# Kernel tuning notes

Hardware: AMD Instinct MI355X
Metric: run time of the kernel (lower is better)

Reference implementation:

```python
import jax, jax.numpy as jnp
import numpy as np

EMBED = 1024
HEADS = 16
HIDDEN = 4 * EMBED
EPS = 1e-5


def layer_norm(x, g, b):
    mu = jnp.mean(x, axis=-1, keepdims=True)
    var = jnp.var(x, axis=-1, keepdims=True)
    return (x - mu) * jax.lax.rsqrt(var + EPS) * g + b


def setup_inputs() -> dict:
    key = jax.random.key(0)
    ks = jax.random.split(key, 8)
    s = EMBED ** -0.5
    return {
        "x": jax.random.normal(ks[0], (4, 2048, EMBED), dtype=jnp.float32),
        "ln1_g": jnp.ones((EMBED,), jnp.float32),
        "ln1_b": jnp.zeros((EMBED,), jnp.float32),
        "qkv_w": jax.random.normal(ks[1], (3 * EMBED, EMBED), jnp.float32) * s,
        "out_w": jax.random.normal(ks[2], (EMBED, EMBED), jnp.float32) * s,
        "out_b": jnp.zeros((EMBED,), jnp.float32),
        "ln2_g": jnp.ones((EMBED,), jnp.float32),
        "ln2_b": jnp.zeros((EMBED,), jnp.float32),
        "fc1_w": jax.random.normal(ks[3], (HIDDEN, EMBED), jnp.float32) * s,
        "fc1_b": jnp.zeros((HIDDEN,), jnp.float32),
        "fc2_w": jax.random.normal(ks[4], (EMBED, HIDDEN), jnp.float32) * (HIDDEN ** -0.5),
        "fc2_b": jnp.zeros((EMBED,), jnp.float32),
    }


def reference(x, ln1_g, ln1_b, qkv_w, out_w, out_b, ln2_g, ln2_b, fc1_w, fc1_b, fc2_w, fc2_b):
    B, N, C = x.shape
    hd = C // HEADS
    # --- attention (pre-LN); note: NO 1/sqrt(d) scaling, matching the source ---
    h = layer_norm(x, ln1_g, ln1_b)
    qkv = h @ qkv_w.T                                  # [B,N,3C]
    qkv = qkv.reshape(B, N, 3, HEADS, hd).transpose(2, 0, 3, 1, 4)
    q, k, v = qkv[0], qkv[1], qkv[2]                   # [B,H,N,hd]
    attn = jax.nn.softmax(jnp.einsum("bhqd,bhkd->bhqk", q, k), axis=-1)
    o = jnp.einsum("bhqk,bhkd->bhqd", attn, v)
    o = o.transpose(0, 2, 1, 3).reshape(B, N, C)
    x = x + o @ out_w.T + out_b
    # --- MLP (exact erf GELU, matching nn.GELU default) ---
    h = layer_norm(x, ln2_g, ln2_b)
    h = jax.nn.gelu(h @ fc1_w.T + fc1_b, approximate=False)
    x = x + h @ fc2_w.T + fc2_b
    return x
```

## Files before the change

### kernel.cpp

```cpp
#include <hip/hip_runtime.h>
#include <cstdint>


using short8 = __attribute__((ext_vector_type(8))) short;
using f32x4  = __attribute__((ext_vector_type(4))) float;
using f32x16 = __attribute__((ext_vector_type(16))) float;

#define EMBED  1024
#define HIDDEN 4096
#define SEQ    2048
#define NTOK   8192

__device__ __forceinline__ ushort f2bf(float x) {
  union { float f; uint32_t u; } v; v.f = x;
  uint32_t r = v.u + 0x7fffu + ((v.u >> 16) & 1u);
  return (ushort)(r >> 16);
}

__device__ __forceinline__ uint32_t pkbf(float lo, float hi) {
  uint32_t r;
  asm("v_cvt_pk_bf16_f32 %0, %1, %2" : "=v"(r) : "v"(lo), "v"(hi));
  return r;
}

__device__ __forceinline__ void gload16(const void* g, void* l) {
  __builtin_amdgcn_global_load_lds((__attribute__((address_space(1))) void*)(g),
                                   (__attribute__((address_space(3))) void*)(l), 16, 0, 0);
}

template<int N> __device__ __forceinline__ void vwait() {
  asm volatile("s_waitcnt vmcnt(%0)" :: "n"(N) : "memory");
}
__device__ __forceinline__ void fence_bar() {
  asm volatile("" ::: "memory");
  __builtin_amdgcn_s_barrier();
  asm volatile("" ::: "memory");
}

__device__ __forceinline__ f32x4 mfma16(short8 a, short8 b, f32x4 c) {
  return __builtin_amdgcn_mfma_f32_16x16x32_bf16(a, b, c, 0, 0, 0);
}
__device__ __forceinline__ f32x16 mfma32(short8 a, short8 b, f32x16 c) {
  return __builtin_amdgcn_mfma_f32_32x32x16_bf16(a, b, c, 0, 0, 0);
}
__device__ __forceinline__ f32x16 zero16() {
  f32x16 z = {0.f,0.f,0.f,0.f,0.f,0.f,0.f,0.f,0.f,0.f,0.f,0.f,0.f,0.f,0.f,0.f};
  return z;
}

__global__ __launch_bounds__(256) void cvt_bf16_kernel(const float* __restrict__ in,
                                                       ushort* __restrict__ out, int n4) {
  int i = blockIdx.x * 256 + threadIdx.x;
  if (i < n4) {
    float4 v = reinterpret_cast<const float4*>(in)[i];
    ushort4 o; o.x = f2bf(v.x); o.y = f2bf(v.y); o.z = f2bf(v.z); o.w = f2bf(v.w);
    reinterpret_cast<ushort4*>(out)[i] = o;
  }
}

__global__ __launch_bounds__(256) void ln_kernel(const float* __restrict__ x,
                                                 const float* __restrict__ g,
                                                 const float* __restrict__ b,
                                                 ushort* __restrict__ out) {
  const int row = blockIdx.x, tid = threadIdx.x;
  const float4 xv = reinterpret_cast<const float4*>(x + (size_t)row * EMBED)[tid];
  float s  = xv.x + xv.y + xv.z + xv.w;
  float s2 = xv.x*xv.x + xv.y*xv.y + xv.z*xv.z + xv.w*xv.w;
  #pragma unroll
  for (int off = 32; off >= 1; off >>= 1) { s += __shfl_xor(s, off); s2 += __shfl_xor(s2, off); }
  __shared__ float ps[4], ps2[4];
  if ((tid & 63) == 0) { ps[tid >> 6] = s; ps2[tid >> 6] = s2; }
  __syncthreads();
  s  = ps[0] + ps[1] + ps[2] + ps[3];
  s2 = ps2[0] + ps2[1] + ps2[2] + ps2[3];
  const float mu  = s * (1.f / EMBED);
  const float var = s2 * (1.f / EMBED) - mu * mu;
  const float rs  = rsqrtf(var + 1e-5f);
  const float4 gv = reinterpret_cast<const float4*>(g)[tid];
  const float4 bv = reinterpret_cast<const float4*>(b)[tid];
  ushort4 o;
  o.x = f2bf((xv.x - mu) * rs * gv.x + bv.x);
  o.y = f2bf((xv.y - mu) * rs * gv.y + bv.y);
  o.z = f2bf((xv.z - mu) * rs * gv.z + bv.z);
  o.w = f2bf((xv.w - mu) * rs * gv.w + bv.w);
  reinterpret_cast<ushort4*>(out + (size_t)row * EMBED)[tid] = o;
}

template<int EPI, bool SQ>
__global__ __launch_bounds__(512) void gemm256(const ushort* __restrict__ A,
                                               const ushort* __restrict__ B,
                                               const float* __restrict__ bias,
                                               const float* __restrict__ res,
                                               ushort* __restrict__ outb,
                                               float* __restrict__ outf,
                                               int M, int N, int K, int gx) {
  constexpr int BN   = SQ ? 256 : 128;
  constexpr int MP   = SQ ? 8 : 4;
  constexpr int NPH  = SQ ? 2 : 1;
  constexpr int LPT  = SQ ? 4 : 3;
  constexpr int NB   = LPT - 2;
  constexpr int ABUF = 256 * 32;
  constexpr int BBUF = BN * 32;
  __shared__ ushort lds[4][ABUF + BBUF];

  const int nwg = gridDim.x;
  const int b0  = blockIdx.x;
  const int p = b0 & 7, li = b0 >> 3;
  int mt, nt;
  if ((gx & 7) == 0) {
    const int g = gx >> 3;
    mt = p * g + (li % g);
    nt = li / g;
  } else {
    const int g = (nwg / gx) >> 3;
    nt = p * g + (li % g);
    mt = li / g;
  }
  const int m0 = mt * 256;
  const int n0 = nt * BN;

  const int tid = threadIdx.x, lane = tid & 63, wave = tid >> 6;
  const int wm = (SQ ? (wave >> 2) : (wave >> 1)) * (MP * 16);
  const int wn = (SQ ? (wave & 3) : (wave & 1)) * 64;
  const int l15 = lane & 15, l4 = lane >> 4;
  const int NT = K >> 5;

  const ushort* aSrc[2];
  const ushort* bSrc[NB];
  #pragma unroll
  for (int rd = 0; rd < 2; ++rd) {
    const int slot = rd * 512 + tid;
    const int r = slot >> 2;
    const int cs = (slot & 3) ^ ((r >> 1) & 3);
    aSrc[rd] = A + (size_t)(m0 + r) * K + cs * 8;
  }
  #pragma unroll
  for (int rd = 0; rd < NB; ++rd) {
    const int slot = rd * 512 + tid;
    const int r = slot >> 2;
    const int cs = (slot & 3) ^ ((r >> 1) & 3);
    bSrc[rd] = B + (size_t)(n0 + r) * K + cs * 8;
  }
  auto stageA = [&](int buf, int rd) { gload16(aSrc[rd], &lds[buf][(rd * 512 + tid) * 8]); };
  auto stageB = [&](int buf, int rd) { gload16(bSrc[rd], &lds[buf][ABUF + (rd * 512 + tid) * 8]); };
  auto advance = [&]() {
    #pragma unroll
    for (int rd = 0; rd < 2; ++rd) aSrc[rd] += 32;
    #pragma unroll
    for (int rd = 0; rd < NB; ++rd) bSrc[rd] += 32;
  };

  #pragma unroll
  for (int t = 0; t < 3; ++t) {
    stageA(t, 0); stageA(t, 1);
    #pragma unroll
    for (int rd = 0; rd < NB; ++rd) stageB(t, rd);
    advance();
  }
  vwait<2 * LPT>();
  fence_bar();

  f32x4 acc[MP][4] = {};

  auto doTile = [&](int q, bool st, int wsel) {
    const ushort* bA = &lds[q][0];
    const ushort* bB = &lds[q][ABUF];
    const int sbuf = (q + 3) & 3;
    short8 bf[4];
    #pragma unroll
    for (int j = 0; j < 4; ++j) {
      const int rb = wn + j * 16 + l15;
      bf[j] = *reinterpret_cast<const short8*>(&bB[rb * 32 + ((l4 ^ ((rb >> 1) & 3)) * 8)]);
    }
    #pragma unroll
    for (int ph = 0; ph < NPH; ++ph) {
      short8 af[4];
      #pragma unroll
      for (int i = 0; i < 4; ++i) {
        const int ra = wm + (ph * 4 + i) * 16 + l15;
        af[i] = *reinterpret_cast<const short8*>(&bA[ra * 32 + ((l4 ^ ((ra >> 1) & 3)) * 8)]);
      }
      if (st) {
        if constexpr (SQ) {
          if (ph == 0) { stageA(sbuf, 0); stageA(sbuf, 1); }
          else         { stageB(sbuf, 0); stageB(sbuf, 1); }
        } else {
          stageA(sbuf, 0); stageA(sbuf, 1); stageB(sbuf, 0);
        }
      }
      fence_bar();
      __builtin_amdgcn_s_setprio(1);
      #pragma unroll
      for (int i = 0; i < 4; ++i)
        #pragma unroll
        for (int j = 0; j < 4; ++j)
          acc[ph * 4 + i][j] = mfma16(af[i], bf[j], acc[ph * 4 + i][j]);
      __builtin_amdgcn_s_setprio(0);
      if (ph == NPH - 1) {
        if (st) advance();
        if (wsel == 0)      vwait<2 * LPT>();
        else if (wsel == 1) vwait<LPT>();
        else if (wsel == 2) vwait<0>();
      }
      fence_bar();
    }
  };

  for (int u0 = 0; u0 < NT - 4; u0 += 4) {
    doTile(0, true, 0); doTile(1, true, 0); doTile(2, true, 0); doTile(3, true, 0);
  }
  doTile(0, true, 0); doTile(1, false, 1); doTile(2, false, 2); doTile(3, false, 3);

  #pragma unroll
  for (int i = 0; i < MP; ++i)
    #pragma unroll
    for (int j = 0; j < 4; ++j)
      #pragma unroll
      for (int r = 0; r < 4; ++r) {
        const int row = m0 + wm + i * 16 + l4 * 4 + r;
        const int col = n0 + wn + j * 16 + l15;
        const size_t idx = (size_t)row * N + col;
        float v = acc[i][j][r];
        if constexpr (EPI == 0) {
          outb[idx] = f2bf(v);
        } else if constexpr (EPI == 1) {
          outf[idx] = v + bias[col] + res[idx];
        } else {
          v += bias[col];
          v = 0.5f * v * (1.f + erff(v * 0.70710678118654752f));
          outb[idx] = f2bf(v);
        }
      }
}

#define KVB 64
#define NTT (SEQ / KVB)

__global__ __launch_bounds__(256, 2) void attn_kernel(const ushort* __restrict__ qk,
                                                      const ushort* __restrict__ vt,
                                                      ushort* __restrict__ outp) {
  const int tid = threadIdx.x, lane = tid & 63, wq = tid >> 6;
  const int hi = lane >> 5, lo = lane & 31;
  const int b = blockIdx.x >> 4, h = blockIdx.x & 15;
  const int q0 = blockIdx.y * 256;

  __shared__ ushort sK[2][64 * 64];
  __shared__ ushort sVt[2][64 * 64];
  __shared__ float sBc[4][2][32];

  short8 qf[2][4];
  #pragma unroll
  for (int s = 0; s < 2; ++s)
    #pragma unroll
    for (int kc = 0; kc < 4; ++kc)
      qf[s][kc] = *reinterpret_cast<const short8*>(
          qk + (size_t)(b * SEQ + q0 + wq * 64 + s * 32 + lo) * 2048 + h * 64 + kc * 16 + hi * 8);

  auto STAGE = [&](int bb, int kt) {
    #pragma unroll
    for (int i = 0; i < 2; ++i) {
      const int slot = i * 256 + tid;
      const int r = slot >> 3;
      const int c = (slot & 7) ^ (r & 7);
      gload16(qk + (size_t)(b * SEQ + kt + r) * 2048 + 1024 + h * 64 + c * 8,
              &sK[bb][(i * 256 + wq * 64) * 8]);
      gload16(vt + (size_t)(h * 64 + r) * 8192 + b * SEQ + kt + c * 8,
              &sVt[bb][(i * 256 + wq * 64) * 8]);
    }
  };

  f32x16 acc[2][2];
  #pragma unroll
  for (int s = 0; s < 2; ++s) { acc[s][0] = zero16(); acc[s][1] = zero16(); }
  float mst[2] = {-1e30f, -1e30f}, lst[2] = {0.f, 0.f};

  STAGE(0, 0);
  for (int t = 0; t < NTT; ++t) {
    const int cur = t & 1;
    __syncthreads();
    if (t + 1 < NTT) STAGE(cur ^ 1, (t + 1) * KVB);

    short8 kf[2][4];
    #pragma unroll
    for (int kvb = 0; kvb < 2; ++kvb)
      #pragma unroll
      for (int kc = 0; kc < 4; ++kc) {
        const int row = kvb * 32 + lo, ch = kc * 2 + hi;
        kf[kvb][kc] = *reinterpret_cast<const short8*>(
            &sK[cur][(row * 8 + (ch ^ (row & 7))) * 8]);
      }

    short8 pa[2][4];
    #pragma unroll
    for (int s = 0; s < 2; ++s) {
      f32x16 st[2];
      #pragma unroll
      for (int kvb = 0; kvb < 2; ++kvb) {
        f32x16 tq = zero16();
        tq = mfma32(kf[kvb][0], qf[s][0], tq);
        tq = mfma32(kf[kvb][1], qf[s][1], tq);
        tq = mfma32(kf[kvb][2], qf[s][2], tq);
        tq = mfma32(kf[kvb][3], qf[s][3], tq);
        st[kvb] = tq;
      }
      float pm = fmaxf(st[0][0], st[0][1]);
      #pragma unroll
      for (int r = 2; r < 16; ++r) pm = fmaxf(pm, st[0][r]);
      #pragma unroll
      for (int r = 0; r < 16; ++r) pm = fmaxf(pm, st[1][r]);
      pm = fmaxf(pm, __shfl_xor(pm, 32));
      if (__any(pm > mst[s] + 8.f)) {
        const float mn = fmaxf(mst[s], pm);
        const float al = __expf(mst[s] - mn);
        mst[s] = mn; lst[s] *= al;
        sBc[wq][s][lo] = al;
        asm volatile("s_waitcnt lgkmcnt(0)" ::: "memory");
        #pragma unroll
        for (int g = 0; g < 4; ++g) {
          const f32x4 a4 = *reinterpret_cast<const f32x4*>(&sBc[wq][s][g * 8 + hi * 4]);
          #pragma unroll
          for (int j = 0; j < 4; ++j) {
            acc[s][0][g * 4 + j] *= a4[j];
            acc[s][1][g * 4 + j] *= a4[j];
          }
        }
      }
      #pragma unroll
      for (int kvb = 0; kvb < 2; ++kvb)
        #pragma unroll
        for (int r = 0; r < 16; ++r)
          st[kvb][r] = __expf(st[kvb][r] - mst[s]);
      {
        const f32x16 sv = st[0] + st[1];
        float sum = ((sv[0] + sv[1]) + (sv[2] + sv[3])) + ((sv[4] + sv[5]) + (sv[6] + sv[7]))
                  + ((sv[8] + sv[9]) + (sv[10] + sv[11])) + ((sv[12] + sv[13]) + (sv[14] + sv[15]));
        sum += __shfl_xor(sum, 32);
        lst[s] += sum;
      }
      #pragma unroll
      for (int kvb = 0; kvb < 2; ++kvb)
        #pragma unroll
        for (int f = 0; f < 2; ++f) {
          uint32_t wa = pkbf(st[kvb][f * 8 + 0], st[kvb][f * 8 + 1]);
          uint32_t wb = pkbf(st[kvb][f * 8 + 2], st[kvb][f * 8 + 3]);
          uint32_t wc = pkbf(st[kvb][f * 8 + 4], st[kvb][f * 8 + 5]);
          uint32_t wd = pkbf(st[kvb][f * 8 + 6], st[kvb][f * 8 + 7]);
          asm volatile("v_permlane32_swap_b32 %0, %1" : "+v"(wa), "+v"(wc));
          asm volatile("v_permlane32_swap_b32 %0, %1" : "+v"(wb), "+v"(wd));
          union { uint32_t w[4]; short8 v; } u;
          u.w[0] = wa; u.w[1] = wb; u.w[2] = wc; u.w[3] = wd;
          pa[s][kvb * 2 + f] = u.v;
        }
    }

    #pragma unroll
    for (int db = 0; db < 2; ++db) {
      short8 vb[4];
      #pragma unroll
      for (int k4 = 0; k4 < 4; ++k4) {
        const int row = db * 32 + lo, ch = k4 * 2 + hi;
        vb[k4] = *reinterpret_cast<const short8*>(
            &sVt[cur][(row * 8 + (ch ^ (row & 7))) * 8]);
      }
      #pragma unroll
      for (int s = 0; s < 2; ++s) {
        acc[s][db] = mfma32(pa[s][0], vb[0], acc[s][db]);
        acc[s][db] = mfma32(pa[s][1], vb[1], acc[s][db]);
        acc[s][db] = mfma32(pa[s][2], vb[2], acc[s][db]);
        acc[s][db] = mfma32(pa[s][3], vb[3], acc[s][db]);
      }
    }
  }

  #pragma unroll
  for (int s = 0; s < 2; ++s) sBc[wq][s][lo] = 1.f / lst[s];
  asm volatile("s_waitcnt lgkmcnt(0)" ::: "memory");
  #pragma unroll
  for (int s = 0; s < 2; ++s)
    #pragma unroll
    for (int g = 0; g < 4; ++g) {
      const f32x4 r4 = *reinterpret_cast<const f32x4*>(&sBc[wq][s][g * 8 + hi * 4]);
      #pragma unroll
      for (int j = 0; j < 4; ++j) {
        const int qrow = q0 + wq * 64 + s * 32 + g * 8 + hi * 4 + j;
        #pragma unroll
        for (int db = 0; db < 2; ++db)
          outp[(size_t)(b * SEQ + qrow) * EMBED + h * 64 + db * 32 + lo] =
              f2bf(acc[s][db][g * 4 + j] * r4[j]);
      }
    }
}

extern "C" void kernel_launch(void* const* d_in, const int* in_sizes, int n_in,
                              void* d_out, int out_size, void* d_ws, size_t ws_size,
                              hipStream_t stream) {
  const float* x     = (const float*)d_in[0];
  const float* ln1_g = (const float*)d_in[1];
  const float* ln1_b = (const float*)d_in[2];
  const float* qkv_w = (const float*)d_in[3];
  const float* out_w = (const float*)d_in[4];
  const float* out_b = (const float*)d_in[5];
  const float* ln2_g = (const float*)d_in[6];
  const float* ln2_b = (const float*)d_in[7];
  const float* fc1_w = (const float*)d_in[8];
  const float* fc1_b = (const float*)d_in[9];
  const float* fc2_w = (const float*)d_in[10];
  const float* fc2_b = (const float*)d_in[11];
  float* out = (float*)d_out;
  char* ws = (char*)d_ws;

  ushort* qkvw = (ushort*)(ws);
  ushort* outw = (ushort*)(ws + 6291456);
  ushort* fc1w = (ushort*)(ws + 8388608);
  ushort* fc2w = (ushort*)(ws + 16777216);
  float*  x1   = (float*) (ws + 25165824);
  ushort* hbuf = (ushort*)(ws + 58720256);
  ushort* qkbuf= (ushort*)(ws + 75497472);
  ushort* vtbuf= (ushort*)(ws + 109051904);
  ushort* obuf = (ushort*)(ws + 125829120);
  ushort* gbuf = qkbuf;

  cvt_bf16_kernel<<<3072, 256, 0, stream>>>(qkv_w, qkvw, 3 * EMBED * EMBED / 4);
  cvt_bf16_kernel<<<1024, 256, 0, stream>>>(out_w, outw, EMBED * EMBED / 4);
  cvt_bf16_kernel<<<4096, 256, 0, stream>>>(fc1_w, fc1w, HIDDEN * EMBED / 4);
  cvt_bf16_kernel<<<4096, 256, 0, stream>>>(fc2_w, fc2w, EMBED * HIDDEN / 4);

  ln_kernel<<<NTOK, 256, 0, stream>>>(x, ln1_g, ln1_b, hbuf);
  gemm256<0, true><<<256, 512, 0, stream>>>(hbuf, qkvw, nullptr, nullptr,
                                            qkbuf, nullptr, NTOK, 2 * EMBED, EMBED, 32);
  gemm256<0, false><<<256, 512, 0, stream>>>(qkvw + 2048 * 1024, hbuf, nullptr, nullptr,
                                             vtbuf, nullptr, EMBED, NTOK, EMBED, 4);
  attn_kernel<<<dim3(64, 8), 256, 0, stream>>>(qkbuf, vtbuf, obuf);
  gemm256<1, false><<<256, 512, 0, stream>>>(obuf, outw, out_b, x,
                                             nullptr, x1, NTOK, EMBED, EMBED, 32);
  ln_kernel<<<NTOK, 256, 0, stream>>>(x1, ln2_g, ln2_b, hbuf);
  gemm256<2, true><<<512, 512, 0, stream>>>(hbuf, fc1w, fc1_b, nullptr,
                                            gbuf, nullptr, NTOK, HIDDEN, EMBED, 32);
  gemm256<1, false><<<256, 512, 0, stream>>>(gbuf, fc2w, fc2_b, x1,
                                             nullptr, out, NTOK, EMBED, HIDDEN, 32);
}
```

Measured before the change: 385.9 us.

## Split attention work across 8 waves with 32 query rows each

The attention kernel moves from 4 waves handling 64 query rows each to 8 waves handling 32 rows each, in 512-thread blocks with launch bounds (512,4). Each wave now keeps half the accumulators and Q fragments, which lowers register pressure and raises resident waves for latency hiding. The K/V tile loads are spread over more threads, so each thread issues one load per buffer instead of two. In exchange, every K/V fragment read from LDS now feeds fewer MFMAs, so LDS read traffic per FLOP doubles, and more waves synchronize at each barrier.

```diff
diff --git a/kernel.cpp b/kernel.cpp
--- a/kernel.cpp
+++ b/kernel.cpp
@@ -30,6 +30,9 @@
 
 template<int N> __device__ __forceinline__ void vwait() {
   asm volatile("s_waitcnt vmcnt(%0)" :: "n"(N) : "memory");
+}
+__device__ __forceinline__ void lgkm0() {
+  asm volatile("s_waitcnt lgkmcnt(0)" ::: "memory");
 }
 __device__ __forceinline__ void fence_bar() {
   asm volatile("" ::: "memory");
@@ -236,7 +239,7 @@
 #define KVB 64
 #define NTT (SEQ / KVB)
 
-__global__ __launch_bounds__(256, 2) void attn_kernel(const ushort* __restrict__ qk,
+__global__ __launch_bounds__(512, 4) void attn_kernel(const ushort* __restrict__ qk,
                                                       const ushort* __restrict__ vt,
                                                       ushort* __restrict__ outp) {
   const int tid = threadIdx.x, lane = tid & 63, wq = tid >> 6;
@@ -246,33 +249,26 @@
 
   __shared__ ushort sK[2][64 * 64];
   __shared__ ushort sVt[2][64 * 64];
-  __shared__ float sBc[4][2][32];
-
-  short8 qf[2][4];
-  #pragma unroll
-  for (int s = 0; s < 2; ++s)
-    #pragma unroll
-    for (int kc = 0; kc < 4; ++kc)
-      qf[s][kc] = *reinterpret_cast<const short8*>(
-          qk + (size_t)(b * SEQ + q0 + wq * 64 + s * 32 + lo) * 2048 + h * 64 + kc * 16 + hi * 8);
+  __shared__ float sBc[8][32];
+
+  short8 qf[4];
+  #pragma unroll
+  for (int kc = 0; kc < 4; ++kc)
+    qf[kc] = *reinterpret_cast<const short8*>(
+        qk + (size_t)(b * SEQ + q0 + wq * 32 + lo) * 2048 + h * 64 + kc * 16 + hi * 8);
 
   auto STAGE = [&](int bb, int kt) {
-    #pragma unroll
-    for (int i = 0; i < 2; ++i) {
-      const int slot = i * 256 + tid;
-      const int r = slot >> 3;
-      const int c = (slot & 7) ^ (r & 7);
-      gload16(qk + (size_t)(b * SEQ + kt + r) * 2048 + 1024 + h * 64 + c * 8,
-              &sK[bb][(i * 256 + wq * 64) * 8]);
-      gload16(vt + (size_t)(h * 64 + r) * 8192 + b * SEQ + kt + c * 8,
-              &sVt[bb][(i * 256 + wq * 64) * 8]);
-    }
+    const int r = tid >> 3;
+    const int c = (tid & 7) ^ (r & 7);
+    gload16(qk + (size_t)(b * SEQ + kt + r) * 2048 + 1024 + h * 64 + c * 8,
+            &sK[bb][wq * 64 * 8]);
+    gload16(vt + (size_t)(h * 64 + r) * 8192 + b * SEQ + kt + c * 8,
+            &sVt[bb][wq * 64 * 8]);
   };
 
-  f32x16 acc[2][2];
-  #pragma unroll
-  for (int s = 0; s < 2; ++s) { acc[s][0] = zero16(); acc[s][1] = zero16(); }
-  float mst[2] = {-1e30f, -1e30f}, lst[2] = {0.f, 0.f};
+  f32x16 acc[2];
+  acc[0] = zero16(); acc[1] = zero16();
+  float mst = -1e30f, lst = 0.f;
 
   STAGE(0, 0);
   for (int t = 0; t < NTT; ++t) {
@@ -290,68 +286,65 @@
             &sK[cur][(row * 8 + (ch ^ (row & 7))) * 8]);
       }
 
-    short8 pa[2][4];
-    #pragma unroll
-    for (int s = 0; s < 2; ++s) {
-      f32x16 st[2];
-      #pragma unroll
-      for (int kvb = 0; kvb < 2; ++kvb) {
-        f32x16 tq = zero16();
-        tq = mfma32(kf[kvb][0], qf[s][0], tq);
-        tq = mfma32(kf[kvb][1], qf[s][1], tq);
-        tq = mfma32(kf[kvb][2], qf[s][2], tq);
-        tq = mfma32(kf[kvb][3], qf[s][3], tq);
-        st[kvb] = tq;
-      }
-      float pm = fmaxf(st[0][0], st[0][1]);
-      #pragma unroll
-      for (int r = 2; r < 16; ++r) pm = fmaxf(pm, st[0][r]);
-      #pragma unroll
-      for (int r = 0; r < 16; ++r) pm = fmaxf(pm, st[1][r]);
-      pm = fmaxf(pm, __shfl_xor(pm, 32));
-      if (__any(pm > mst[s] + 8.f)) {
-        const float mn = fmaxf(mst[s], pm);
-        const float al = __expf(mst[s] - mn);
-        mst[s] = mn; lst[s] *= al;
-        sBc[wq][s][lo] = al;
-        asm volatile("s_waitcnt lgkmcnt(0)" ::: "memory");
+    f32x16 st[2];
+    #pragma unroll
+    for (int kvb = 0; kvb < 2; ++kvb) {
+      f32x16 tq = zero16();
+      tq = mfma32(kf[kvb][0], qf[0], tq);
+      tq = mfma32(kf[kvb][1], qf[1], tq);
+      tq = mfma32(kf[kvb][2], qf[2], tq);
+      tq = mfma32(kf[kvb][3], qf[3], tq);
+      st[kvb] = tq;
+    }
+    float pm = fmaxf(st[0][0], st[0][1]);
+    #pragma unroll
+    for (int r = 2; r < 16; ++r) pm = fmaxf(pm, st[0][r]);
+    #pragma unroll
+    for (int r = 0; r < 16; ++r) pm = fmaxf(pm, st[1][r]);
+    pm = fmaxf(pm, __shfl_xor(pm, 32));
+    if (__any(pm > mst + 8.f)) {
+      const float mn = fmaxf(mst, pm);
+      const float al = __expf(mst - mn);
+      mst = mn; lst *= al;
+      sBc[wq][lo] = al;
+      lgkm0();
+      #pragma unroll
+      for (int g = 0; g < 4; ++g) {
+        const f32x4 a4 = *reinterpret_cast<const f32x4*>(&sBc[wq][g * 8 + hi * 4]);
         #pragma unroll
-        for (int g = 0; g < 4; ++g) {
-          const f32x4 a4 = *reinterpret_cast<const f32x4*>(&sBc[wq][s][g * 8 + hi * 4]);
-          #pragma unroll
-          for (int j = 0; j < 4; ++j) {
-            acc[s][0][g * 4 + j] *= a4[j];
-            acc[s][1][g * 4 + j] *= a4[j];
-          }
+        for (int j = 0; j < 4; ++j) {
+          acc[0][g * 4 + j] *= a4[j];
+          acc[1][g * 4 + j] *= a4[j];
         }
       }
-      #pragma unroll
-      for (int kvb = 0; kvb < 2; ++kvb)
-        #pragma unroll
-        for (int r = 0; r < 16; ++r)
-          st[kvb][r] = __expf(st[kvb][r] - mst[s]);
-      {
-        const f32x16 sv = st[0] + st[1];
-        float sum = ((sv[0] + sv[1]) + (sv[2] + sv[3])) + ((sv[4] + sv[5]) + (sv[6] + sv[7]))
-                  + ((sv[8] + sv[9]) + (sv[10] + sv[11])) + ((sv[12] + sv[13]) + (sv[14] + sv[15]));
-        sum += __shfl_xor(sum, 32);
-        lst[s] += sum;
-      }
-      #pragma unroll
-      for (int kvb = 0; kvb < 2; ++kvb)
-        #pragma unroll
-        for (int f = 0; f < 2; ++f) {
-          uint32_t wa = pkbf(st[kvb][f * 8 + 0], st[kvb][f * 8 + 1]);
-          uint32_t wb = pkbf(st[kvb][f * 8 + 2], st[kvb][f * 8 + 3]);
-          uint32_t wc = pkbf(st[kvb][f * 8 + 4], st[kvb][f * 8 + 5]);
-          uint32_t wd = pkbf(st[kvb][f * 8 + 6], st[kvb][f * 8 + 7]);
-          asm volatile("v_permlane32_swap_b32 %0, %1" : "+v"(wa), "+v"(wc));
-          asm volatile("v_permlane32_swap_b32 %0, %1" : "+v"(wb), "+v"(wd));
-          union { uint32_t w[4]; short8 v; } u;
-          u.w[0] = wa; u.w[1] = wb; u.w[2] = wc; u.w[3] = wd;
-          pa[s][kvb * 2 + f] = u.v;
-        }
-    }
+    }
+    #pragma unroll
+    for (int kvb = 0; kvb < 2; ++kvb)
+      #pragma unroll
+      for (int r = 0; r < 16; ++r)
+        st[kvb][r] = __expf(st[kvb][r] - mst);
+    {
+      const f32x16 sv = st[0] + st[1];
+      float sum = ((sv[0] + sv[1]) + (sv[2] + sv[3])) + ((sv[4] + sv[5]) + (sv[6] + sv[7]))
+                + ((sv[8] + sv[9]) + (sv[10] + sv[11])) + ((sv[12] + sv[13]) + (sv[14] + sv[15]));
+      sum += __shfl_xor(sum, 32);
+      lst += sum;
+    }
+    short8 pa[4];
+    #pragma unroll
+    for (int kvb = 0; kvb < 2; ++kvb)
+      #pragma unroll
+      for (int f = 0; f < 2; ++f) {
+        uint32_t wa = pkbf(st[kvb][f * 8 + 0], st[kvb][f * 8 + 1]);
+        uint32_t wb = pkbf(st[kvb][f * 8 + 2], st[kvb][f * 8 + 3]);
+        uint32_t wc = pkbf(st[kvb][f * 8 + 4], st[kvb][f * 8 + 5]);
+        uint32_t wd = pkbf(st[kvb][f * 8 + 6], st[kvb][f * 8 + 7]);
+        asm volatile("v_permlane32_swap_b32 %0, %1" : "+v"(wa), "+v"(wc));
+        asm volatile("v_permlane32_swap_b32 %0, %1" : "+v"(wb), "+v"(wd));
+        union { uint32_t w[4]; short8 v; } u;
+        u.w[0] = wa; u.w[1] = wb; u.w[2] = wc; u.w[3] = wd;
+        pa[kvb * 2 + f] = u.v;
+      }
 
     #pragma unroll
     for (int db = 0; db < 2; ++db) {
@@ -362,33 +355,27 @@
         vb[k4] = *reinterpret_cast<const short8*>(
             &sVt[cur][(row * 8 + (ch ^ (row & 7))) * 8]);
       }
-      #pragma unroll
-      for (int s = 0; s < 2; ++s) {
-        acc[s][db] = mfma32(pa[s][0], vb[0], acc[s][db]);
-        acc[s][db] = mfma32(pa[s][1], vb[1], acc[s][db]);
-        acc[s][db] = mfma32(pa[s][2], vb[2], acc[s][db]);
-        acc[s][db] = mfma32(pa[s][3], vb[3], acc[s][db]);
-      }
-    }
-  }
-
-  #pragma unroll
-  for (int s = 0; s < 2; ++s) sBc[wq][s][lo] = 1.f / lst[s];
-  asm volatile("s_waitcnt lgkmcnt(0)" ::: "memory");
-  #pragma unroll
-  for (int s = 0; s < 2; ++s)
-    #pragma unroll
-    for (int g = 0; g < 4; ++g) {
-      const f32x4 r4 = *reinterpret_cast<const f32x4*>(&sBc[wq][s][g * 8 + hi * 4]);
-      #pragma unroll
-      for (int j = 0; j < 4; ++j) {
-        const int qrow = q0 + wq * 64 + s * 32 + g * 8 + hi * 4 + j;
-        #pragma unroll
-        for (int db = 0; db < 2; ++db)
-          outp[(size_t)(b * SEQ + qrow) * EMBED + h * 64 + db * 32 + lo] =
-              f2bf(acc[s][db][g * 4 + j] * r4[j]);
-      }
-    }
+      acc[db] = mfma32(pa[0], vb[0], acc[db]);
+      acc[db] = mfma32(pa[1], vb[1], acc[db]);
+      acc[db] = mfma32(pa[2], vb[2], acc[db]);
+      acc[db] = mfma32(pa[3], vb[3], acc[db]);
+    }
+  }
+
+  sBc[wq][lo] = 1.f / lst;
+  lgkm0();
+  #pragma unroll
+  for (int g = 0; g < 4; ++g) {
+    const f32x4 r4 = *reinterpret_cast<const f32x4*>(&sBc[wq][g * 8 + hi * 4]);
+    #pragma unroll
+    for (int j = 0; j < 4; ++j) {
+      const int qrow = q0 + wq * 32 + g * 8 + hi * 4 + j;
+      #pragma unroll
+      for (int db = 0; db < 2; ++db)
+        outp[(size_t)(b * SEQ + qrow) * EMBED + h * 64 + db * 32 + lo] =
+            f2bf(acc[db][g * 4 + j] * r4[j]);
+    }
+  }
 }
 
 extern "C" void kernel_launch(void* const* d_in, const int* in_sizes, int n_in,
@@ -430,7 +417,7 @@
                                             qkbuf, nullptr, NTOK, 2 * EMBED, EMBED, 32);
   gemm256<0, false><<<256, 512, 0, stream>>>(qkvw + 2048 * 1024, hbuf, nullptr, nullptr,
                                              vtbuf, nullptr, EMBED, NTOK, EMBED, 4);
-  attn_kernel<<<dim3(64, 8), 256, 0, stream>>>(qkbuf, vtbuf, obuf);
+  attn_kernel<<<dim3(64, 8), 512, 0, stream>>>(qkbuf, vtbuf, obuf);
   gemm256<1, false><<<256, 512, 0, stream>>>(obuf, outw, out_b, x,
                                              nullptr, x1, NTOK, EMBED, EMBED, 32);
   ln_kernel<<<NTOK, 256, 0, stream>>>(x1, ln2_g, ln2_b, hbuf);
```

New measurement: 384.5 us. No clear change (-0.4%).
